# Performance work log

Hardware: AMD Instinct MI355X
Metric: run time of the kernel (lower is better)

Reference implementation:

```python
import jax, jax.numpy as jnp
import numpy as np

DIRECTIONAL_WEIGHT = 0.85
MAGNITUDE_WEIGHT = 0.15
TREND_WEIGHT = 0.1
EPS = 1e-8

B = 8388608
C = 3


def setup_inputs() -> dict:
    key = jax.random.key(0)
    k1, k2, k3, k4 = jax.random.split(key, 4)
    predictions = jax.random.normal(k1, (B, C), dtype=jnp.float32)
    targets = jax.random.randint(k2, (B,), 0, C, dtype=jnp.int32)
    price_changes = jax.random.normal(k3, (B,), dtype=jnp.float32)
    trend_direction = jax.random.normal(k4, (B,), dtype=jnp.float32)
    return {
        "predictions": predictions,
        "targets": targets,
        "price_changes": price_changes,
        "trend_direction": trend_direction,
    }


def reference(predictions, targets, price_changes, trend_direction):
    # per-sample cross entropy (reduction='none')
    logp = jax.nn.log_softmax(predictions, axis=1)  # [B, C]
    ce_loss = -jnp.take_along_axis(logp, targets[:, None].astype(jnp.int32), axis=1)[:, 0]  # [B]

    # magnitude weighting
    magnitude_weights = jnp.abs(price_changes)
    magnitude_weights = magnitude_weights / (magnitude_weights.mean() + EPS)
    weighted_ce = ce_loss * magnitude_weights

    # vectorized trend alignment (replaces the python loop)
    up_aligned = (trend_direction > 0) & (targets == 2)
    down_aligned = (trend_direction < 0) & (targets == 0)
    trend_alignment = jnp.where(up_aligned | down_aligned, -0.1, 0.0).astype(ce_loss.dtype)

    total_loss = (
        DIRECTIONAL_WEIGHT * weighted_ce.mean()
        + MAGNITUDE_WEIGHT * ce_loss.mean()
        + TREND_WEIGHT * trend_alignment.mean()
    )
    return total_loss
```

## Files before the change

### kernel.cpp

```cpp
#include <hip/hip_runtime.h>

#define B_TOTAL   8388608
#define NQUADS    (B_TOTAL / 4)
#define THREADS   256
#define BLOCKS    2048
#define NTHREADS  (BLOCKS * THREADS)
#define UNROLL    (NQUADS / NTHREADS)

__global__ __launch_bounds__(THREADS, 4) void trading_loss_fused(
    const float* __restrict__ preds,
    const int*   __restrict__ targets,
    const float* __restrict__ pc,
    const float* __restrict__ td,
    float*        __restrict__ sums,
    unsigned int* __restrict__ count,
    float*        __restrict__ out)
{
    const unsigned tid = blockIdx.x * THREADS + threadIdx.x;

    const float4* preds4 = reinterpret_cast<const float4*>(preds);
    const int4*   tg4    = reinterpret_cast<const int4*  >(targets);
    const float4* pc4    = reinterpret_cast<const float4*>(pc);
    const float4* td4    = reinterpret_cast<const float4*>(td);

    float4 A0[UNROLL], A1[UNROLL], A2[UNROLL];
    int4   T[UNROLL];
    float4 P[UNROLL], D[UNROLL];

    #pragma unroll
    for (int u = 0; u < UNROLL; ++u) {
        const unsigned q = u * NTHREADS + tid;
        A0[u] = preds4[(size_t)q * 3 + 0];
        A1[u] = preds4[(size_t)q * 3 + 1];
        A2[u] = preds4[(size_t)q * 3 + 2];
        T[u]  = tg4[q];
        P[u]  = pc4[q];
        D[u]  = td4[q];
    }

    float s_cew = 0.f, s_ce = 0.f, s_mw = 0.f, s_tr = 0.f;

    #pragma unroll
    for (int u = 0; u < UNROLL; ++u) {
        float p[12] = {A0[u].x, A0[u].y, A0[u].z, A0[u].w,
                       A1[u].x, A1[u].y, A1[u].z, A1[u].w,
                       A2[u].x, A2[u].y, A2[u].z, A2[u].w};
        int   tt[4]  = {T[u].x, T[u].y, T[u].z, T[u].w};
        float pcv[4] = {P[u].x, P[u].y, P[u].z, P[u].w};
        float tdv[4] = {D[u].x, D[u].y, D[u].z, D[u].w};

        #pragma unroll
        for (int j = 0; j < 4; ++j) {
            float p0 = p[j*3 + 0], p1 = p[j*3 + 1], p2 = p[j*3 + 2];
            float m  = fmaxf(fmaxf(p0, p1), p2);
            float e0 = __expf(p0 - m);
            float e1 = __expf(p1 - m);
            float e2 = __expf(p2 - m);
            float lse = __logf(e0 + e1 + e2);
            int   t  = tt[j];
            float pt = (t == 0) ? p0 : ((t == 1) ? p1 : p2);
            float ce = lse - (pt - m);
            float aw = fabsf(pcv[j]);

            s_ce  += ce;
            s_cew += ce * aw;
            s_mw  += aw;
            bool aligned = (tdv[j] > 0.f && t == 2) || (tdv[j] < 0.f && t == 0);
            s_tr += aligned ? 1.0f : 0.0f;
        }
    }

    #pragma unroll
    for (int off = 32; off >= 1; off >>= 1) {
        s_cew += __shfl_down(s_cew, off, 64);
        s_ce  += __shfl_down(s_ce , off, 64);
        s_mw  += __shfl_down(s_mw , off, 64);
        s_tr  += __shfl_down(s_tr , off, 64);
    }

    __shared__ float red[4][4];
    const int lane = threadIdx.x & 63;
    const int wave = threadIdx.x >> 6;
    if (lane == 0) {
        red[wave][0] = s_cew;
        red[wave][1] = s_ce;
        red[wave][2] = s_mw;
        red[wave][3] = s_tr;
    }
    __syncthreads();

    if (threadIdx.x == 0) {
        float r0 = red[0][0] + red[1][0] + red[2][0] + red[3][0];
        float r1 = red[0][1] + red[1][1] + red[2][1] + red[3][1];
        float r2 = red[0][2] + red[1][2] + red[2][2] + red[3][2];
        float r3 = red[0][3] + red[1][3] + red[2][3] + red[3][3];

        atomicAdd(&sums[0], r0);
        atomicAdd(&sums[1], r1);
        atomicAdd(&sums[2], r2);
        atomicAdd(&sums[3], r3);

        __threadfence();
        unsigned old = atomicAdd(count, 1u);
        if (old == BLOCKS - 1) {
            float cew = atomicAdd(&sums[0], 0.0f);
            float ce  = atomicAdd(&sums[1], 0.0f);
            float mw  = atomicAdd(&sums[2], 0.0f);
            float tr  = atomicAdd(&sums[3], 0.0f);

            const float invB = 1.0f / (float)B_TOTAL;
            float cew_mean = cew * invB;
            float ce_mean  = ce  * invB;
            float mw_mean  = mw  * invB + 1e-8f;
            float tr_mean  = -0.1f * tr * invB;
            out[0] = 0.85f * (cew_mean / mw_mean) + 0.15f * ce_mean + 0.1f * tr_mean;
        }
    }
}

extern "C" void kernel_launch(void* const* d_in, const int* in_sizes, int n_in,
                              void* d_out, int out_size, void* d_ws, size_t ws_size,
                              hipStream_t stream) {
    const float* preds   = (const float*)d_in[0];
    const int*   targets = (const int*  )d_in[1];
    const float* pc      = (const float*)d_in[2];
    const float* td      = (const float*)d_in[3];
    float* out  = (float*)d_out;
    float* sums = (float*)d_ws;
    unsigned int* count = (unsigned int*)((char*)d_ws + 4 * sizeof(float));

    hipMemsetAsync(d_ws, 0, 5 * sizeof(float), stream);

    trading_loss_fused<<<BLOCKS, THREADS, 0, stream>>>(preds, targets, pc, td,
                                                       sums, count, out);
}
```

Baseline: 328.0 us.

## Coalesce prediction loads via LDS transpose with per-wave prefetch

Each wave now reads a contiguous chunk of the predictions array with unit-stride float4 loads and stages it in shared memory, then reads back each lane's three rows. The loop runs over work items with the next item's loads issued before the current one is computed. The grid is doubled and the occupancy hint removed. This adds two block barriers per iteration and extra LDS traffic in exchange for fully coalesced global accesses.

```diff
diff --git a/kernel.cpp b/kernel.cpp
--- a/kernel.cpp
+++ b/kernel.cpp
@@ -1,13 +1,15 @@
 #include <hip/hip_runtime.h>
 
 #define B_TOTAL   8388608
-#define NQUADS    (B_TOTAL / 4)
 #define THREADS   256
-#define BLOCKS    2048
-#define NTHREADS  (BLOCKS * THREADS)
-#define UNROLL    (NQUADS / NTHREADS)
+#define BLOCKS    4096
+#define WPB       4
+#define GW_TOTAL  (BLOCKS * WPB)
+#define SPWI      256
+#define WI_TOTAL  (B_TOTAL / SPWI)
+#define ITERS     (WI_TOTAL / GW_TOTAL)
 
-__global__ __launch_bounds__(THREADS, 4) void trading_loss_fused(
+__global__ __launch_bounds__(THREADS) void trading_loss_fused(
     const float* __restrict__ preds,
     const int*   __restrict__ targets,
     const float* __restrict__ pc,
@@ -16,38 +18,56 @@
     unsigned int* __restrict__ count,
     float*        __restrict__ out)
 {
-    const unsigned tid = blockIdx.x * THREADS + threadIdx.x;
+    const int wave = threadIdx.x >> 6;
+    const int l    = threadIdx.x & 63;
+    const int gw   = blockIdx.x * WPB + wave;
 
     const float4* preds4 = reinterpret_cast<const float4*>(preds);
     const int4*   tg4    = reinterpret_cast<const int4*  >(targets);
     const float4* pc4    = reinterpret_cast<const float4*>(pc);
     const float4* td4    = reinterpret_cast<const float4*>(td);
 
-    float4 A0[UNROLL], A1[UNROLL], A2[UNROLL];
-    int4   T[UNROLL];
-    float4 P[UNROLL], D[UNROLL];
-
-    #pragma unroll
-    for (int u = 0; u < UNROLL; ++u) {
-        const unsigned q = u * NTHREADS + tid;
-        A0[u] = preds4[(size_t)q * 3 + 0];
-        A1[u] = preds4[(size_t)q * 3 + 1];
-        A2[u] = preds4[(size_t)q * 3 + 2];
-        T[u]  = tg4[q];
-        P[u]  = pc4[q];
-        D[u]  = td4[q];
-    }
+    __shared__ float4 stage[WPB][192];
+    float4* st = stage[wave];
 
     float s_cew = 0.f, s_ce = 0.f, s_mw = 0.f, s_tr = 0.f;
 
+    int wi = gw;
+    float4 A0 = preds4[(size_t)wi * 192 +   0 + l];
+    float4 A1 = preds4[(size_t)wi * 192 +  64 + l];
+    float4 A2 = preds4[(size_t)wi * 192 + 128 + l];
+    int4   T  = tg4[(size_t)wi * 64 + l];
+    float4 P  = pc4[(size_t)wi * 64 + l];
+    float4 D  = td4[(size_t)wi * 64 + l];
+
     #pragma unroll
-    for (int u = 0; u < UNROLL; ++u) {
-        float p[12] = {A0[u].x, A0[u].y, A0[u].z, A0[u].w,
-                       A1[u].x, A1[u].y, A1[u].z, A1[u].w,
-                       A2[u].x, A2[u].y, A2[u].z, A2[u].w};
-        int   tt[4]  = {T[u].x, T[u].y, T[u].z, T[u].w};
-        float pcv[4] = {P[u].x, P[u].y, P[u].z, P[u].w};
-        float tdv[4] = {D[u].x, D[u].y, D[u].z, D[u].w};
+    for (int it = 0; it < ITERS; ++it) {
+        __syncthreads();
+        st[  0 + l] = A0;
+        st[ 64 + l] = A1;
+        st[128 + l] = A2;
+
+        float4 nA0, nA1, nA2, nP, nD; int4 nT;
+        const int nwi = wi + GW_TOTAL;
+        if (it + 1 < ITERS) {
+            nA0 = preds4[(size_t)nwi * 192 +   0 + l];
+            nA1 = preds4[(size_t)nwi * 192 +  64 + l];
+            nA2 = preds4[(size_t)nwi * 192 + 128 + l];
+            nT  = tg4[(size_t)nwi * 64 + l];
+            nP  = pc4[(size_t)nwi * 64 + l];
+            nD  = td4[(size_t)nwi * 64 + l];
+        }
+
+        __syncthreads();
+
+        float4 r0 = st[3*l + 0];
+        float4 r1 = st[3*l + 1];
+        float4 r2 = st[3*l + 2];
+
+        float p[12] = {r0.x,r0.y,r0.z,r0.w, r1.x,r1.y,r1.z,r1.w, r2.x,r2.y,r2.z,r2.w};
+        int   tt[4]  = {T.x, T.y, T.z, T.w};
+        float pcv[4] = {P.x, P.y, P.z, P.w};
+        float tdv[4] = {D.x, D.y, D.z, D.w};
 
         #pragma unroll
         for (int j = 0; j < 4; ++j) {
@@ -68,6 +88,11 @@
             bool aligned = (tdv[j] > 0.f && t == 2) || (tdv[j] < 0.f && t == 0);
             s_tr += aligned ? 1.0f : 0.0f;
         }
+
+        if (it + 1 < ITERS) {
+            A0 = nA0; A1 = nA1; A2 = nA2; T = nT; P = nP; D = nD;
+            wi = nwi;
+        }
     }
 
     #pragma unroll
@@ -78,10 +103,8 @@
         s_tr  += __shfl_down(s_tr , off, 64);
     }
 
-    __shared__ float red[4][4];
-    const int lane = threadIdx.x & 63;
-    const int wave = threadIdx.x >> 6;
-    if (lane == 0) {
+    __shared__ float red[WPB][4];
+    if (l == 0) {
         red[wave][0] = s_cew;
         red[wave][1] = s_ce;
         red[wave][2] = s_mw;
```

Measured after the change: 443.6 us. +35.2%, slower.
